# Performance work log

Hardware: AMD Instinct MI355X
Metric: run time of the kernel (lower is better)

The kernel has to match this reference:

```python
import jax, jax.numpy as jnp
import numpy as np

B, N, C = 2, 30, 320
FH = FW = 64          # feature map (latent 128 / downsample 2)
PH = PW = 32          # roi_scale output size at this level
ORIG = 128.0          # original (latent) spatial size
SCALE = 0.5           # spatial_scale = 1/downsample_rate
SR = 2                # sampling_ratio
M = N + 1             # global channel + rois


def _bilinear(img, y, x):
    # img: (C, H, W); y, x: arbitrary-shape float coords. torchvision-style:
    # zero outside [-1, H]/[ -1, W], clamp then 4-corner interp.
    H, W = img.shape[1], img.shape[2]
    valid = (y > -1.0) & (y < H) & (x > -1.0) & (x < W)
    yc = jnp.clip(y, 0.0, H - 1.0)
    xc = jnp.clip(x, 0.0, W - 1.0)
    y0 = jnp.floor(yc).astype(jnp.int32)
    x0 = jnp.floor(xc).astype(jnp.int32)
    y1 = jnp.minimum(y0 + 1, H - 1)
    x1 = jnp.minimum(x0 + 1, W - 1)
    wy = yc - y0
    wx = xc - x0
    v = (img[:, y0, x0] * (1 - wy) * (1 - wx)
         + img[:, y0, x1] * (1 - wy) * wx
         + img[:, y1, x0] * wy * (1 - wx)
         + img[:, y1, x1] * wy * wx)
    return v * valid


def _roi_align_one(img, x1, y1, bw, bh):
    # img (C,FH,FW); x1,y1,bw,bh (N,) in aligned feature coords / bin sizes
    s = (jnp.arange(PH * SR, dtype=img.dtype) + 0.5) / SR   # sub-sample offsets in bin units
    yy = y1[:, None] + s[None, :] * bh[:, None]             # (N, PH*SR)
    xx = x1[:, None] + s[None, :] * bw[:, None]             # (N, PW*SR)
    yg = jnp.broadcast_to(yy[:, :, None], (N, PH * SR, PW * SR))
    xg = jnp.broadcast_to(xx[:, None, :], (N, PH * SR, PW * SR))
    v = _bilinear(img, yg, xg)                              # (C, N, PH*SR, PW*SR)
    v = v.reshape(C, N, PH, SR, PW, SR).mean(axis=(3, 5))   # average sub-samples
    return v.transpose(1, 0, 2, 3)                          # (N, C, PH, PW)


def _roi_unpool_one(roi_imgs, x1, y1, bw, bh):
    # inverse of roi_align: paste each (C,PH,PW) roi back into its own (FH,FW) map
    ys = jnp.arange(FH, dtype=roi_imgs.dtype)
    xs = jnp.arange(FW, dtype=roi_imgs.dtype)
    ry = (ys[None, :] - y1[:, None]) / bh[:, None] - 0.5    # (N, FH) roi-grid coords
    rx = (xs[None, :] - x1[:, None]) / bw[:, None] - 0.5    # (N, FW)
    ryg = jnp.broadcast_to(ry[:, :, None], (N, FH, FW))
    rxg = jnp.broadcast_to(rx[:, None, :], (N, FH, FW))
    return jax.vmap(_bilinear)(roi_imgs, ryg, rxg)          # (N, C, FH, FW); zeros outside box


def _fuser(x, perm, w_reduce, w1, b1, w2, b2):
    # FuseWeightGenerator: x (B, M, C, H, W)
    fg = jnp.sum(x, axis=2) != 0                            # (B, M, H, W) foreground mask
    fw = jnp.einsum('bmchw,c->bmhw', x, w_reduce)           # 1x1 conv C->1, no bias
    g = fw[:, :1]
    r = fw[:, 1:][:, perm]                                  # shuffle roi channels
    gin = jnp.concatenate([g, r], axis=1)                   # (B, M, H, W)
    # ChannelGate: only the 'max' branch affects the output (original uses last channel_att_raw)
    mp = gin.max(axis=(2, 3))                               # (B, M)
    att = jax.nn.relu(mp @ w1 + b1) @ w2 + b2
    gated = gin * jax.nn.sigmoid(att)[:, :, None, None]
    inv = jnp.argsort(perm)
    fw = jnp.concatenate([gated[:, :1], gated[:, 1:][:, inv]], axis=1)
    fw = jnp.where(fg, fw, jnp.finfo(fw.dtype).min)
    w = jax.nn.softmax(fw, axis=1)[:, :, None]              # (B, M, 1, H, W)
    return jnp.sum(x * w, axis=1)                           # (B, C, H, W)


def _forward(normed_hidden_states, attn_output, instance_boxes, instance_masks, perm,
             w_reduce, w1, b1, w2, b2):
    fmap = normed_hidden_states.reshape(B, FH, FW, C).transpose(0, 3, 1, 2)  # b c h w
    boxes = instance_boxes * ORIG * SCALE - 0.5             # aligned=True feature coords
    x1, y1 = boxes[..., 0], boxes[..., 1]
    x2, y2 = boxes[..., 2], boxes[..., 3]
    bw = (x2 - x1) / PW
    bh = (y2 - y1) / PH
    roi_feats = jax.vmap(_roi_align_one)(fmap, x1, y1, bw, bh)   # (B,N,C,PH,PW)
    mask = instance_masks.astype(roi_feats.dtype)[:, :, None, None, None]
    roi_feats = roi_feats * mask                             # masked rois stay zero
    unpooled = jax.vmap(_roi_unpool_one)(roi_feats, x1, y1, bw, bh) * mask  # (B,N,C,FH,FW)
    attn_map = attn_output.reshape(B, FH, FW, C).transpose(0, 3, 1, 2)[:, None]
    x = jnp.concatenate([attn_map, unpooled], axis=1)        # (B, M, C, FH, FW)
    fused = _fuser(x, perm, w_reduce, w1, b1, w2, b2)        # (B, C, FH, FW)
    return fused.transpose(0, 2, 3, 1).reshape(B, FH * FW, C)


def setup_inputs() -> dict:
    key = jax.random.key(0)
    ks = jax.random.split(key, 10)
    nhs = jax.random.normal(ks[0], (B, FH * FW, C), dtype=jnp.float32)
    attn = jax.random.normal(ks[1], (B, FH * FW, C), dtype=jnp.float32)
    cx = jax.random.uniform(ks[2], (B, N), minval=0.25, maxval=0.75)
    cy = jax.random.uniform(ks[3], (B, N), minval=0.25, maxval=0.75)
    hw = jax.random.uniform(ks[4], (B, N, 2), minval=0.1, maxval=0.4)
    boxes = jnp.stack([cx - hw[..., 0] / 2, cy - hw[..., 1] / 2,
                       cx + hw[..., 0] / 2, cy + hw[..., 1] / 2], axis=-1)
    boxes = jnp.clip(boxes, 0.0, 1.0).astype(jnp.float32)    # normalized xyxy
    masks = jax.random.randint(ks[5], (B, N), 0, 2).astype(jnp.int32)
    perm = jax.random.permutation(ks[6], N).astype(jnp.int32)
    w_reduce = (jax.random.normal(ks[7], (C,), dtype=jnp.float32) / np.sqrt(C)).astype(jnp.float32)
    w1 = (jax.random.normal(ks[8], (M, M), dtype=jnp.float32) / np.sqrt(M)).astype(jnp.float32)
    b1 = jnp.zeros((M,), dtype=jnp.float32)
    w2 = (jax.random.normal(ks[9], (M, M), dtype=jnp.float32) / np.sqrt(M)).astype(jnp.float32)
    b2 = jnp.zeros((M,), dtype=jnp.float32)
    return {"normed_hidden_states": nhs, "attn_output": attn, "instance_boxes": boxes,
            "instance_masks": masks, "perm": perm, "w_reduce": w_reduce,
            "w1": w1, "b1": b1, "w2": w2, "b2": b2}


def reference(normed_hidden_states, attn_output, instance_boxes, instance_masks, perm,
              w_reduce, w1, b1, w2, b2):
    return _forward(normed_hidden_states, attn_output, instance_boxes, instance_masks, perm,
                    w_reduce, w1, b1, w2, b2)
```

## Files before the change

### kernel.cpp

```cpp
#include <hip/hip_runtime.h>
#include <hip/hip_bf16.h>

#define NB 2
#define NN 30
#define NC 320
#define NM 31
#define HW 4096
#define FMIN_F (-3.40282346638528859812e+38f)

typedef float nfloat4 __attribute__((ext_vector_type(4)));

#define OFF_FSUM   0
#define OFF_FWRED  8192
#define OFF_ASUM   16384
#define OFF_AWRED  24576
#define OFF_Z      32768
#define OFF_MP     286720
#define WS_FLOATS  286784

#define GRID_ROIF (NB * NN * 128)
#define GRID_RED  1639

__device__ __forceinline__ void get_box(const float* boxes, int b, int n,
                                        float& x1, float& y1, float& bw, float& bh) {
    const float* p = boxes + (b * NN + n) * 4;
    float X1 = p[0] * 64.0f - 0.5f;
    float Y1 = p[1] * 64.0f - 0.5f;
    float X2 = p[2] * 64.0f - 0.5f;
    float Y2 = p[3] * 64.0f - 0.5f;
    x1 = X1; y1 = Y1;
    bw = (X2 - X1) / 32.0f;
    bh = (Y2 - Y1) / 32.0f;
}

__device__ __forceinline__ unsigned short f2bf(float f) {
    __hip_bfloat16 h = __float2bfloat16(f);
    return *reinterpret_cast<unsigned short*>(&h);
}
__device__ __forceinline__ unsigned pack2(float a, float b) {
    return (unsigned)f2bf(a) | ((unsigned)f2bf(b) << 16);
}
__device__ __forceinline__ float blo(unsigned u) { return __uint_as_float(u << 16); }
__device__ __forceinline__ float bhi(unsigned u) { return __uint_as_float(u & 0xffff0000u); }

__device__ void do_roifeat(int blk, const float* __restrict__ nhs,
                           const float* __restrict__ boxes,
                           const int* __restrict__ masks,
                           unsigned* __restrict__ roif) {
    int bn = blk >> 7;
    int n = bn % NN;
    int b = bn / NN;
    if (masks[b * NN + n] == 0) return;
    __shared__ float wsm[8][9];
    __shared__ int bsm[8];
    int tid = threadIdx.x;
    float x1, y1, bw, bh;
    get_box(boxes, b, n, x1, y1, bw, bh);

    if (tid < 8) {
        int cell = blk * 8 + tid;
        int q = cell & 31;
        int p = (cell >> 5) & 31;
        float W[9] = {0.f,0.f,0.f,0.f,0.f,0.f,0.f,0.f,0.f};
        float wys[4], wxs[4];
        int iy0s[4], ix0s[4];
        int iymin = 64, ixmin = 64;
#pragma unroll
        for (int s_ = 0; s_ < 4; s_++) {
            int di = s_ >> 1, dj = s_ & 1;
            float y = y1 + ((float)p + 0.25f + 0.5f * (float)di) * bh;
            float x = x1 + ((float)q + 0.25f + 0.5f * (float)dj) * bw;
            float yc = fminf(fmaxf(y, 0.0f), 63.0f);
            float xc = fminf(fmaxf(x, 0.0f), 63.0f);
            int iy0 = (int)floorf(yc), ix0 = (int)floorf(xc);
            wys[s_] = yc - (float)iy0;
            wxs[s_] = xc - (float)ix0;
            iy0s[s_] = iy0; ix0s[s_] = ix0;
            iymin = min(iymin, iy0); ixmin = min(ixmin, ix0);
        }
#pragma unroll
        for (int s_ = 0; s_ < 4; s_++) {
            float wy = wys[s_], wx = wxs[s_];
            int dy = iy0s[s_] - iymin;
            int dx = ix0s[s_] - ixmin;
            bool yt = (iy0s[s_] == 63);
            bool xt = (ix0s[s_] == 63);
            float ay0 = yt ? 1.0f : (1.0f - wy);
            float ay1 = yt ? 0.0f : wy;
            float ax0 = xt ? 1.0f : (1.0f - wx);
            float ax1 = xt ? 0.0f : wx;
            float r0 = dy ? 0.0f : ay0;
            float r1 = dy ? ay0  : ay1;
            float r2 = dy ? ay1  : 0.0f;
            float c0 = dx ? 0.0f : ax0;
            float c1 = dx ? ax0  : ax1;
            float c2 = dx ? ax1  : 0.0f;
            W[0] += r0 * c0; W[1] += r0 * c1; W[2] += r0 * c2;
            W[3] += r1 * c0; W[4] += r1 * c1; W[5] += r1 * c2;
            W[6] += r2 * c0; W[7] += r2 * c1; W[8] += r2 * c2;
        }
#pragma unroll
        for (int k = 0; k < 9; k++) wsm[tid][k] = W[k] * 0.25f;
        bsm[tid] = iymin * 64 + ixmin;
    }
    __syncthreads();

    int cid = tid / 40;
    int v = tid - cid * 40;
    int cell = blk * 8 + cid;
    const float4* fb4 = (const float4*)(nhs + (size_t)b * HW * NC);
    int base = bsm[cid];
    float4 acc0 = make_float4(0.f, 0.f, 0.f, 0.f);
    float4 acc1 = make_float4(0.f, 0.f, 0.f, 0.f);
#pragma unroll
    for (int i = 0; i < 3; i++) {
#pragma unroll
        for (int j = 0; j < 3; j++) {
            float w = wsm[cid][i * 3 + j];
            if (w != 0.0f) {
                int off = (base + i * 64 + j) * 80 + v * 2;
                float4 f0 = fb4[off];
                float4 f1 = fb4[off + 1];
                acc0.x += w * f0.x; acc0.y += w * f0.y;
                acc0.z += w * f0.z; acc0.w += w * f0.w;
                acc1.x += w * f1.x; acc1.y += w * f1.y;
                acc1.z += w * f1.z; acc1.w += w * f1.w;
            }
        }
    }
    uint4 pk;
    pk.x = pack2(acc0.x, acc0.y);
    pk.y = pack2(acc0.z, acc0.w);
    pk.z = pack2(acc1.x, acc1.y);
    pk.w = pack2(acc1.z, acc1.w);
    ((uint4*)roif)[(size_t)cell * 40 + v] = pk;
}

__device__ void do_reduce(int rblk, const float* __restrict__ nhs,
                          const float* __restrict__ attn,
                          const float* __restrict__ wred, float* __restrict__ ws) {
    int wave = threadIdx.x >> 6;
    int lane = threadIdx.x & 63;
    int row = rblk * 5 + wave;
    if (row >= NB * HW) return;
    const float4* n4 = (const float4*)(nhs + (size_t)row * NC);
    const float4* a4 = (const float4*)(attn + (size_t)row * NC);
    const float4* w4 = (const float4*)wred;
    float4 wv = w4[lane];
    float4 nv = n4[lane];
    float4 av = a4[lane];
    float s_n = nv.x + nv.y + nv.z + nv.w;
    float w_n = nv.x * wv.x + nv.y * wv.y + nv.z * wv.z + nv.w * wv.w;
    float s_a = av.x + av.y + av.z + av.w;
    float w_a = av.x * wv.x + av.y * wv.y + av.z * wv.z + av.w * wv.w;
    if (lane < 16) {
        float4 wv2 = w4[lane + 64];
        float4 nv2 = n4[lane + 64];
        float4 av2 = a4[lane + 64];
        s_n += nv2.x + nv2.y + nv2.z + nv2.w;
        w_n += nv2.x * wv2.x + nv2.y * wv2.y + nv2.z * wv2.z + nv2.w * wv2.w;
        s_a += av2.x + av2.y + av2.z + av2.w;
        w_a += av2.x * wv2.x + av2.y * wv2.y + av2.z * wv2.z + av2.w * wv2.w;
    }
#pragma unroll
    for (int off = 32; off > 0; off >>= 1) {
        s_n += __shfl_down(s_n, off, 64);
        w_n += __shfl_down(w_n, off, 64);
        s_a += __shfl_down(s_a, off, 64);
        w_a += __shfl_down(w_a, off, 64);
    }
    if (lane == 0) {
        ws[OFF_FSUM + row]  = s_n;
        ws[OFF_FWRED + row] = w_n;
        ws[OFF_ASUM + row]  = s_a;
        ws[OFF_AWRED + row] = w_a;
    }
}

__global__ void k_stage1(const float* __restrict__ nhs, const float* __restrict__ attn,
                         const float* __restrict__ boxes, const int* __restrict__ masks,
                         const float* __restrict__ wred, float* __restrict__ ws,
                         unsigned* __restrict__ roif) {
    int blk = blockIdx.x;
    if (blk < GRID_ROIF) {
        do_roifeat(blk, nhs, boxes, masks, roif);
    } else {
        do_reduce(blk - GRID_ROIF, nhs, attn, wred, ws);
    }
}

__global__ void k_fw(const float* __restrict__ boxes, const int* __restrict__ masks,
                     float* __restrict__ ws) {
    int bm = blockIdx.x;
    int b = bm / NM, m = bm % NM;
    __shared__ float rs[1024], rw[1024];
    __shared__ float red[256];
    float locmax = -INFINITY;
    int tid = threadIdx.x;
    if (m == 0) {
        for (int pix = tid; pix < HW; pix += 256) {
            float fwv = ws[OFF_AWRED + b * HW + pix];
            bool fg = (ws[OFF_ASUM + b * HW + pix] != 0.0f);
            ws[OFF_Z + (size_t)bm * HW + pix] = fg ? fwv : FMIN_F;
            locmax = fmaxf(locmax, fwv);
        }
    } else {
        int n = m - 1;
        int msk = masks[b * NN + n];
        if (msk) {
            float x1, y1, bw, bh;
            get_box(boxes, b, n, x1, y1, bw, bh);
            const float* fsum  = ws + OFF_FSUM + b * HW;
            const float* fwred = ws + OFF_FWRED + b * HW;
            for (int cell = tid; cell < 1024; cell += 256) {
                int q = cell & 31, p = cell >> 5;
                float accs = 0.f, accw = 0.f;
#pragma unroll
                for (int di = 0; di < 2; di++) {
#pragma unroll
                    for (int dj = 0; dj < 2; dj++) {
                        float y = y1 + ((float)p + 0.25f + 0.5f * (float)di) * bh;
                        float x = x1 + ((float)q + 0.25f + 0.5f * (float)dj) * bw;
                        float yc = fminf(fmaxf(y, 0.0f), 63.0f);
                        float xc = fminf(fmaxf(x, 0.0f), 63.0f);
                        int iy0 = (int)floorf(yc), ix0 = (int)floorf(xc);
                        int iy1 = min(iy0 + 1, 63), ix1 = min(ix0 + 1, 63);
                        float wy = yc - (float)iy0, wx = xc - (float)ix0;
                        float w00 = (1.f - wy) * (1.f - wx), w01 = (1.f - wy) * wx;
                        float w10 = wy * (1.f - wx), w11 = wy * wx;
                        accs += w00 * fsum[iy0 * 64 + ix0] + w01 * fsum[iy0 * 64 + ix1]
                              + w10 * fsum[iy1 * 64 + ix0] + w11 * fsum[iy1 * 64 + ix1];
                        accw += w00 * fwred[iy0 * 64 + ix0] + w01 * fwred[iy0 * 64 + ix1]
                              + w10 * fwred[iy1 * 64 + ix0] + w11 * fwred[iy1 * 64 + ix1];
                    }
                }
                rs[cell] = accs * 0.25f;
                rw[cell] = accw * 0.25f;
            }
            __syncthreads();
            for (int pix = tid; pix < HW; pix += 256) {
                int h = pix >> 6, wp = pix & 63;
                float fwv = 0.0f;
                bool fg = false;
                float ry = ((float)h - y1) / bh - 0.5f;
                float rx = ((float)wp - x1) / bw - 0.5f;
                bool valid = (ry > -1.0f) && (ry < 32.0f) && (rx > -1.0f) && (rx < 32.0f);
                if (valid) {
                    float yc = fminf(fmaxf(ry, 0.0f), 31.0f);
                    float xc = fminf(fmaxf(rx, 0.0f), 31.0f);
                    int iy0 = (int)floorf(yc), ix0 = (int)floorf(xc);
                    int iy1 = min(iy0 + 1, 31), ix1 = min(ix0 + 1, 31);
                    float wy = yc - (float)iy0, wx = xc - (float)ix0;
                    float w00 = (1.f - wy) * (1.f - wx), w01 = (1.f - wy) * wx;
                    float w10 = wy * (1.f - wx), w11 = wy * wx;
                    fwv = w00 * rw[iy0 * 32 + ix0] + w01 * rw[iy0 * 32 + ix1]
                        + w10 * rw[iy1 * 32 + ix0] + w11 * rw[iy1 * 32 + ix1];
                    float su = w00 * rs[iy0 * 32 + ix0] + w01 * rs[iy0 * 32 + ix1]
                             + w10 * rs[iy1 * 32 + ix0] + w11 * rs[iy1 * 32 + ix1];
                    fg = (su != 0.0f);
                }
                ws[OFF_Z + (size_t)bm * HW + pix] = fg ? fwv : FMIN_F;
                locmax = fmaxf(locmax, fwv);
            }
        } else {
            for (int pix = tid; pix < HW; pix += 256)
                ws[OFF_Z + (size_t)bm * HW + pix] = FMIN_F;
            locmax = 0.0f;
        }
    }
    red[tid] = locmax;
    __syncthreads();
    for (int s = 128; s > 0; s >>= 1) {
        if (tid < s) red[tid] = fmaxf(red[tid], red[tid + s]);
        __syncthreads();
    }
    if (tid == 0) ws[OFF_MP + bm] = red[0];
}

__global__ void k_final(const float* __restrict__ attn, const float* __restrict__ boxes,
                        const int* __restrict__ perm, const float* __restrict__ w1,
                        const float* __restrict__ b1, const float* __restrict__ w2,
                        const float* __restrict__ b2, const float* __restrict__ ws,
                        const unsigned* __restrict__ roif, float* __restrict__ out) {
    __shared__ float mpg[NM], hb[NM], scal[32], wbuf[8][32];
    int t = threadIdx.x;
    int idx0 = blockIdx.x * 8;
    int b = idx0 >> 12;

    if (t < NM) {
        mpg[t] = (t == 0) ? ws[OFF_MP + b * NM]
                          : ws[OFF_MP + b * NM + 1 + perm[t - 1]];
    }
    __syncthreads();
    if (t < NM) {
        float a = b1[t];
#pragma unroll
        for (int k = 0; k < NM; k++) a += mpg[k] * w1[k * NM + t];
        hb[t] = fmaxf(a, 0.0f);
    }
    __syncthreads();
    if (t < NM) {
        float a = b2[t];
#pragma unroll
        for (int k = 0; k < NM; k++) a += hb[k] * w2[k * NM + t];
        float sig = 1.0f / (1.0f + expf(-a));
        if (t == 0) scal[0] = sig;
        else        scal[1 + perm[t - 1]] = sig;
    }
    __syncthreads();

    if (t < 256) {
        int pg = t >> 5, m = t & 31;
        int pix = (idx0 + pg) & 4095;
        float zz = FMIN_F;
        if (m < NM) {
            float v = ws[OFF_Z + (size_t)(b * NM + m) * HW + pix];
            zz = (v == FMIN_F) ? FMIN_F : v * scal[m];
        }
        float mx = zz;
#pragma unroll
        for (int off = 16; off > 0; off >>= 1)
            mx = fmaxf(mx, __shfl_xor(mx, off, 64));
        float e = (m < NM) ? expf(zz - mx) : 0.0f;
        float s = e;
#pragma unroll
        for (int off = 16; off > 0; off >>= 1)
            s += __shfl_xor(s, off, 64);
        if (m < NM) wbuf[pg][m] = e / s;
    }
    __syncthreads();

    int pid = t / 40;
    int v = t - pid * 40;
    int idx = idx0 + pid;
    int pix = idx & 4095;
    int h = pix >> 6, wp = pix & 63;
    float w0 = wbuf[pid][0];
    const float4* at4 = (const float4*)attn;
    float4 a0 = at4[(size_t)idx * 80 + v * 2];
    float4 a1 = at4[(size_t)idx * 80 + v * 2 + 1];
    float4 acc0, acc1;
    acc0.x = a0.x * w0; acc0.y = a0.y * w0; acc0.z = a0.z * w0; acc0.w = a0.w * w0;
    acc1.x = a1.x * w0; acc1.y = a1.y * w0; acc1.z = a1.z * w0; acc1.w = a1.w * w0;
    const uint4* r4 = (const uint4*)roif;
    for (int n = 0; n < NN; n++) {
        float wn = wbuf[pid][n + 1];
        if (wn == 0.0f) continue;
        float x1, y1, bw, bh;
        get_box(boxes, b, n, x1, y1, bw, bh);
        float ry = ((float)h - y1) / bh - 0.5f;
        float rx = ((float)wp - x1) / bw - 0.5f;
        float yc = fminf(fmaxf(ry, 0.0f), 31.0f);
        float xc = fminf(fmaxf(rx, 0.0f), 31.0f);
        int iy0 = (int)floorf(yc), ix0 = (int)floorf(xc);
        int iy1 = min(iy0 + 1, 31), ix1 = min(ix0 + 1, 31);
        float wy = yc - (float)iy0, wx = xc - (float)ix0;
        float w00 = (1.f - wy) * (1.f - wx) * wn, w01 = (1.f - wy) * wx * wn;
        float w10 = wy * (1.f - wx) * wn, w11 = wy * wx * wn;
        size_t base = ((size_t)(b * NN + n)) << 10;
        uint4 U00 = r4[(base + iy0 * 32 + ix0) * 40 + v];
        uint4 U01 = r4[(base + iy0 * 32 + ix1) * 40 + v];
        uint4 U10 = r4[(base + iy1 * 32 + ix0) * 40 + v];
        uint4 U11 = r4[(base + iy1 * 32 + ix1) * 40 + v];
        acc0.x += w00 * blo(U00.x) + w01 * blo(U01.x) + w10 * blo(U10.x) + w11 * blo(U11.x);
        acc0.y += w00 * bhi(U00.x) + w01 * bhi(U01.x) + w10 * bhi(U10.x) + w11 * bhi(U11.x);
        acc0.z += w00 * blo(U00.y) + w01 * blo(U01.y) + w10 * blo(U10.y) + w11 * blo(U11.y);
        acc0.w += w00 * bhi(U00.y) + w01 * bhi(U01.y) + w10 * bhi(U10.y) + w11 * bhi(U11.y);
        acc1.x += w00 * blo(U00.z) + w01 * blo(U01.z) + w10 * blo(U10.z) + w11 * blo(U11.z);
        acc1.y += w00 * bhi(U00.z) + w01 * bhi(U01.z) + w10 * bhi(U10.z) + w11 * bhi(U11.z);
        acc1.z += w00 * blo(U00.w) + w01 * blo(U01.w) + w10 * blo(U10.w) + w11 * blo(U11.w);
        acc1.w += w00 * bhi(U00.w) + w01 * bhi(U01.w) + w10 * bhi(U10.w) + w11 * bhi(U11.w);
    }
    nfloat4 nv0 = { acc0.x, acc0.y, acc0.z, acc0.w };
    nfloat4 nv1 = { acc1.x, acc1.y, acc1.z, acc1.w };
    __builtin_nontemporal_store(nv0, ((nfloat4*)out) + (size_t)idx * 80 + v * 2);
    __builtin_nontemporal_store(nv1, ((nfloat4*)out) + (size_t)idx * 80 + v * 2 + 1);
}

extern "C" void kernel_launch(void* const* d_in, const int* in_sizes, int n_in,
                              void* d_out, int out_size, void* d_ws, size_t ws_size,
                              hipStream_t stream) {
    const float* nhs   = (const float*)d_in[0];
    const float* attn  = (const float*)d_in[1];
    const float* boxes = (const float*)d_in[2];
    const int*   masks = (const int*)d_in[3];
    const int*   perm  = (const int*)d_in[4];
    const float* wred  = (const float*)d_in[5];
    const float* w1    = (const float*)d_in[6];
    const float* b1    = (const float*)d_in[7];
    const float* w2    = (const float*)d_in[8];
    const float* b2    = (const float*)d_in[9];
    float* out = (float*)d_out;
    float* ws = (float*)d_ws;
    unsigned* roif = (unsigned*)((char*)d_ws + (size_t)WS_FLOATS * 4);

    k_stage1<<<GRID_ROIF + GRID_RED, 320, 0, stream>>>(nhs, attn, boxes, masks, wred, ws, roif);
    k_fw<<<NB * NM, 256, 0, stream>>>(boxes, masks, ws);
    k_final<<<NB * HW / 8, 320, 0, stream>>>(attn, boxes, perm, w1, b1, w2, b2, ws, roif, out);
}
```

Baseline: 119.7 us.

## Split k_fw across pixel chunks with atomic max, compact active ROI list in final

k_fw now launches 8 blocks per (batch, channel), each covering 512 pixels. Each block computes only the ROI rows its chunk needs, and the per-channel maximum is merged with an order-preserving atomicMax on encoded floats, zeroed inside stage1. In k_final, each pixel builds a compacted list of ROIs with nonzero softmax weight, so the loop no longer walks all 30 ROIs with a branch. This adds encode/decode and atomic overhead, and the atomic list order makes the floating-point summation order nondeterministic.

```diff
diff --git a/kernel.cpp b/kernel.cpp
--- a/kernel.cpp
+++ b/kernel.cpp
@@ -7,6 +7,7 @@
 #define NM 31
 #define HW 4096
 #define FMIN_F (-3.40282346638528859812e+38f)
+#define PCH 8
 
 typedef float nfloat4 __attribute__((ext_vector_type(4)));
 
@@ -42,6 +43,15 @@
 }
 __device__ __forceinline__ float blo(unsigned u) { return __uint_as_float(u << 16); }
 __device__ __forceinline__ float bhi(unsigned u) { return __uint_as_float(u & 0xffff0000u); }
+
+__device__ __forceinline__ unsigned encf(float f) {
+    unsigned u = __float_as_uint(f);
+    return (u & 0x80000000u) ? ~u : (u | 0x80000000u);
+}
+__device__ __forceinline__ float decf(unsigned e) {
+    unsigned u = (e & 0x80000000u) ? (e & 0x7fffffffu) : ~e;
+    return __uint_as_float(u);
+}
 
 __device__ void do_roifeat(int blk, const float* __restrict__ nhs,
                            const float* __restrict__ boxes,
@@ -139,6 +149,8 @@
 __device__ void do_reduce(int rblk, const float* __restrict__ nhs,
                           const float* __restrict__ attn,
                           const float* __restrict__ wred, float* __restrict__ ws) {
+    if (rblk == 0 && threadIdx.x < 64)
+        ((unsigned*)(ws + OFF_MP))[threadIdx.x] = 0u;
     int wave = threadIdx.x >> 6;
     int lane = threadIdx.x & 63;
     int row = rblk * 5 + wave;
@@ -191,14 +203,16 @@
 
 __global__ void k_fw(const float* __restrict__ boxes, const int* __restrict__ masks,
                      float* __restrict__ ws) {
-    int bm = blockIdx.x;
+    int bm = blockIdx.x / PCH;
+    int ch = blockIdx.x % PCH;
     int b = bm / NM, m = bm % NM;
+    int pix0 = ch * (HW / PCH);
     __shared__ float rs[1024], rw[1024];
     __shared__ float red[256];
     float locmax = -INFINITY;
     int tid = threadIdx.x;
     if (m == 0) {
-        for (int pix = tid; pix < HW; pix += 256) {
+        for (int pix = pix0 + tid; pix < pix0 + HW / PCH; pix += 256) {
             float fwv = ws[OFF_AWRED + b * HW + pix];
             bool fg = (ws[OFF_ASUM + b * HW + pix] != 0.0f);
             ws[OFF_Z + (size_t)bm * HW + pix] = fg ? fwv : FMIN_F;
@@ -210,10 +224,16 @@
         if (msk) {
             float x1, y1, bw, bh;
             get_box(boxes, b, n, x1, y1, bw, bh);
+            int h0 = pix0 >> 6;
+            float ry_lo = ((float)h0 - y1) / bh - 0.5f;
+            float ry_hi = ((float)(h0 + 7) - y1) / bh - 0.5f;
+            int iy_lo = max(0, (int)floorf(fminf(fmaxf(ry_lo, 0.0f), 31.0f)) - 1);
+            int iy_hi = min(31, (int)floorf(fminf(fmaxf(ry_hi, 0.0f), 31.0f)) + 2);
             const float* fsum  = ws + OFF_FSUM + b * HW;
             const float* fwred = ws + OFF_FWRED + b * HW;
             for (int cell = tid; cell < 1024; cell += 256) {
                 int q = cell & 31, p = cell >> 5;
+                if (p < iy_lo || p > iy_hi) continue;
                 float accs = 0.f, accw = 0.f;
 #pragma unroll
                 for (int di = 0; di < 2; di++) {
@@ -238,7 +258,7 @@
                 rw[cell] = accw * 0.25f;
             }
             __syncthreads();
-            for (int pix = tid; pix < HW; pix += 256) {
+            for (int pix = pix0 + tid; pix < pix0 + HW / PCH; pix += 256) {
                 int h = pix >> 6, wp = pix & 63;
                 float fwv = 0.0f;
                 bool fg = false;
@@ -263,7 +283,7 @@
                 locmax = fmaxf(locmax, fwv);
             }
         } else {
-            for (int pix = tid; pix < HW; pix += 256)
+            for (int pix = pix0 + tid; pix < pix0 + HW / PCH; pix += 256)
                 ws[OFF_Z + (size_t)bm * HW + pix] = FMIN_F;
             locmax = 0.0f;
         }
@@ -274,7 +294,8 @@
         if (tid < s) red[tid] = fmaxf(red[tid], red[tid + s]);
         __syncthreads();
     }
-    if (tid == 0) ws[OFF_MP + bm] = red[0];
+    if (tid == 0)
+        atomicMax((unsigned*)(ws + OFF_MP) + bm, encf(red[0]));
 }
 
 __global__ void k_final(const float* __restrict__ attn, const float* __restrict__ boxes,
@@ -283,13 +304,16 @@
                         const float* __restrict__ b2, const float* __restrict__ ws,
                         const unsigned* __restrict__ roif, float* __restrict__ out) {
     __shared__ float mpg[NM], hb[NM], scal[32], wbuf[8][32];
+    __shared__ int acnt[8];
+    __shared__ unsigned char alist[8][NN];
     int t = threadIdx.x;
     int idx0 = blockIdx.x * 8;
     int b = idx0 >> 12;
 
+    if (t < 8) acnt[t] = 0;
     if (t < NM) {
-        mpg[t] = (t == 0) ? ws[OFF_MP + b * NM]
-                          : ws[OFF_MP + b * NM + 1 + perm[t - 1]];
+        unsigned e = ((const unsigned*)(ws + OFF_MP))[b * NM + ((t == 0) ? 0 : 1 + perm[t - 1])];
+        mpg[t] = decf(e);
     }
     __syncthreads();
     if (t < NM) {
@@ -326,7 +350,14 @@
 #pragma unroll
         for (int off = 16; off > 0; off >>= 1)
             s += __shfl_xor(s, off, 64);
-        if (m < NM) wbuf[pg][m] = e / s;
+        if (m < NM) {
+            float w = e / s;
+            wbuf[pg][m] = w;
+            if (m >= 1 && w != 0.0f) {
+                int pos = atomicAdd(&acnt[pg], 1);
+                alist[pg][pos] = (unsigned char)(m - 1);
+            }
+        }
     }
     __syncthreads();
 
@@ -343,9 +374,10 @@
     acc0.x = a0.x * w0; acc0.y = a0.y * w0; acc0.z = a0.z * w0; acc0.w = a0.w * w0;
     acc1.x = a1.x * w0; acc1.y = a1.y * w0; acc1.z = a1.z * w0; acc1.w = a1.w * w0;
     const uint4* r4 = (const uint4*)roif;
-    for (int n = 0; n < NN; n++) {
+    int na = acnt[pid];
+    for (int k = 0; k < na; k++) {
+        int n = alist[pid][k];
         float wn = wbuf[pid][n + 1];
-        if (wn == 0.0f) continue;
         float x1, y1, bw, bh;
         get_box(boxes, b, n, x1, y1, bw, bh);
         float ry = ((float)h - y1) / bh - 0.5f;
@@ -395,6 +427,6 @@
     unsigned* roif = (unsigned*)((char*)d_ws + (size_t)WS_FLOATS * 4);
 
     k_stage1<<<GRID_ROIF + GRID_RED, 320, 0, stream>>>(nhs, attn, boxes, masks, wred, ws, roif);
-    k_fw<<<NB * NM, 256, 0, stream>>>(boxes, masks, ws);
+    k_fw<<<NB * NM * PCH, 256, 0, stream>>>(boxes, masks, ws);
     k_final<<<NB * HW / 8, 320, 0, stream>>>(attn, boxes, perm, w1, b1, w2, b2, ws, roif, out);
 }
```

Result: no change. 117.4 us (-1.9%).
